# Performance work log

Hardware: AMD Instinct MI355X
Metric: run time of the kernel (lower is better)

## Reference

```python
import jax, jax.numpy as jnp
import numpy as np

D = 768      # embedding_dim
M = 3072     # mlp_dim
G = 4        # num_expert_groups
E = 8        # experts_per_group
KG = 2       # k_groups
KE = 4       # k_experts
EPS = 1e-6   # gate weight threshold from the torch module


def setup_inputs() -> dict:
    key = jax.random.key(0)
    ks = jax.random.split(key, 9)
    x = jax.random.normal(ks[0], (1, 1024, D), dtype=jnp.float32)
    Wg = jax.random.normal(ks[1], (D, G), dtype=jnp.float32) * 0.02
    bg = jax.random.normal(ks[2], (G,), dtype=jnp.float32) * 0.01
    We = jax.random.normal(ks[3], (G, D, E), dtype=jnp.float32) * 0.02
    be = jax.random.normal(ks[4], (G, E), dtype=jnp.float32) * 0.01
    W1 = jax.random.normal(ks[5], (G, E, D, M), dtype=jnp.float32) * 0.02
    b1 = jax.random.normal(ks[6], (G, E, M), dtype=jnp.float32) * 0.01
    W2 = jax.random.normal(ks[7], (G, E, M, D), dtype=jnp.float32) * 0.02
    b2 = jax.random.normal(ks[8], (G, E, D), dtype=jnp.float32) * 0.01
    return {"x": x, "Wg": Wg, "bg": bg, "We": We, "be": be,
            "W1": W1, "b1": b1, "W2": W2, "b2": b2}


def _topk_gates(logits, k):
    # top-k logits -> softmax over the k entries, then zero out weights < 1e-6
    top, idx = jax.lax.top_k(logits, k)
    gates = jax.nn.softmax(top, axis=-1)
    gates = jnp.where(gates >= EPS, gates, jnp.zeros_like(gates))
    return gates, idx


def reference(x, Wg, bg, We, be, W1, b1, W2, b2):
    orig_shape = x.shape
    xf = x.reshape(-1, D)  # [N, D]

    # ---- level 1: group gating (eval mode: clean logits, no noise) ----
    glog = xf @ Wg + bg                      # [N, G]
    ggates, gidx = _topk_gates(glog, KG)     # [N, KG]
    gw = jnp.einsum('nk,nkg->ng', ggates,
                    jax.nn.one_hot(gidx, G, dtype=xf.dtype))  # dense [N, G]

    # ---- level 2: expert gating within each group ----
    # computed densely for all groups; unselected groups get zero group weight
    elog = jnp.einsum('nd,gde->nge', xf, We) + be  # [N, G, E]
    egates, eidx = _topk_gates(elog, KE)            # [N, G, KE]
    ew = jnp.einsum('ngk,ngke->nge', egates,
                    jax.nn.one_hot(eidx, E, dtype=xf.dtype))  # dense [N, G, E]

    combine = gw[:, :, None] * ew  # [N, G, E] combine weights

    # ---- expert MLPs (dense compute, combine-weighted sum) ----
    y = jnp.zeros_like(xf)
    for g in range(G):  # small fixed loop over expert groups
        h = jax.nn.gelu(jnp.einsum('nd,edm->enm', xf, W1[g]) + b1[g][:, None, :],
                        approximate=False)               # [E, N, M]
        o = jnp.einsum('enm,emd->end', h, W2[g]) + b2[g][:, None, :]  # [E, N, D]
        y = y + jnp.einsum('end,ne->nd', o, combine[:, g, :])
    return y.reshape(orig_shape)
```

## Files before the change

### kernel.cpp

```cpp
#include <hip/hip_runtime.h>
#include <hip/hip_bf16.h>
#include <math.h>

#define NTOK 1024
#define DDIM 768
#define MDIM 3072
#define GN 4
#define EN 8
#define NEXP 32
#define NPAIR 8192
#define EPSW 1e-6f

typedef __attribute__((ext_vector_type(4))) float f32x4;
typedef __attribute__((ext_vector_type(4))) int   i32x4;
typedef __attribute__((ext_vector_type(4))) unsigned short u16x4;
typedef __attribute__((ext_vector_type(8))) __bf16 bf16x8;

__device__ __forceinline__ unsigned short f2bf(float f) {
  unsigned u = __builtin_bit_cast(unsigned, f);
  u += 0x7FFFu + ((u >> 16) & 1u);
  return (unsigned short)(u >> 16);
}

__global__ __launch_bounds__(256) void gating_kernel(
    const float* __restrict__ x, const float* __restrict__ Wg,
    const float* __restrict__ bg, const float* __restrict__ We,
    const float* __restrict__ be, int* __restrict__ counts,
    int* __restrict__ pair_e, float* __restrict__ pair_w)
{
  __shared__ float xr[DDIM];
  __shared__ float logits[36];
  const int n = blockIdx.x;
  const int tid = threadIdx.x;
  const float* xp = x + (size_t)n * DDIM;
  for (int d = tid; d < DDIM; d += 256) xr[d] = xp[d];
  __syncthreads();

  const int w = tid >> 6, lane = tid & 63;
  for (int j = 0; j < 9; ++j) {
    const int o = w + 4 * j;
    float s = 0.f;
    if (o < 4) {
      for (int d = lane; d < DDIM; d += 64) s += xr[d] * Wg[d * GN + o];
    } else {
      const int g = (o - 4) >> 3, e = (o - 4) & 7;
      const float* wp = We + (size_t)g * DDIM * EN + e;
      for (int d = lane; d < DDIM; d += 64) s += xr[d] * wp[d * EN];
    }
    for (int off = 32; off; off >>= 1) s += __shfl_xor(s, off);
    if (lane == 0) logits[o] = s + ((o < 4) ? bg[o] : be[o - 4]);
  }
  __syncthreads();

  if (tid == 0) {
    float gl[4];
    for (int i = 0; i < 4; ++i) gl[i] = logits[i];
    int i0 = 0;
    for (int i = 1; i < 4; ++i) if (gl[i] > gl[i0]) i0 = i;
    int i1 = -1;
    for (int i = 0; i < 4; ++i) {
      if (i == i0) continue;
      if (i1 < 0 || gl[i] > gl[i1]) i1 = i;
    }
    const float m = gl[i0];
    const float e1 = expf(gl[i1] - m);
    const float s2 = 1.f + e1;
    float gv[2] = { 1.f / s2, e1 / s2 };
    int gi[2] = { i0, i1 };
    for (int r = 0; r < 2; ++r) if (gv[r] < EPSW) gv[r] = 0.f;

    for (int r = 0; r < 2; ++r) {
      const int g = gi[r];
      float el[8];
      for (int e = 0; e < 8; ++e) el[e] = logits[4 + g * 8 + e];
      int sel[4];
      for (int q = 0; q < 4; ++q) {
        int best = -1;
        for (int e = 0; e < 8; ++e) {
          bool used = false;
          for (int p = 0; p < q; ++p) if (sel[p] == e) used = true;
          if (used) continue;
          if (best < 0 || el[e] > el[best]) best = e;
        }
        sel[q] = best;
      }
      const float mm = el[sel[0]];
      float ex[4]; float ss = 0.f;
      for (int q = 0; q < 4; ++q) { ex[q] = expf(el[sel[q]] - mm); ss += ex[q]; }
      for (int q = 0; q < 4; ++q) {
        float ew = ex[q] / ss;
        if (ew < EPSW) ew = 0.f;
        const int gbl = g * 8 + sel[q];
        const int j = r * 4 + q;
        pair_e[n * 8 + j] = gbl;
        pair_w[n * 8 + j] = gv[r] * ew;
        atomicAdd(&counts[gbl], 1);
      }
    }
  }
}

__global__ void scan_kernel(const int* __restrict__ counts, int* __restrict__ offsets)
{
  if (threadIdx.x == 0) {
    int a = 0;
    for (int i = 0; i < NEXP; ++i) { offsets[i] = a; a += counts[i]; }
  }
}

__global__ __launch_bounds__(256) void scatter_kernel(
    const float* __restrict__ x, const int* __restrict__ pair_e,
    const float* __restrict__ pair_w, const int* __restrict__ offsets,
    int* __restrict__ cursor, int* __restrict__ token_slots,
    float* __restrict__ slot_w, unsigned short* __restrict__ Xg)
{
  __shared__ int slots[8];
  const int n = blockIdx.x, tid = threadIdx.x;
  if (tid < 8) {
    const int e = pair_e[n * 8 + tid];
    const int s = offsets[e] + atomicAdd(&cursor[e], 1);
    slots[tid] = s;
    token_slots[n * 8 + tid] = s;
    slot_w[s] = pair_w[n * 8 + tid];
  }
  __syncthreads();
  const float* xp = x + (size_t)n * DDIM;
  for (int d = tid; d < DDIM; d += 256) {
    const unsigned short h = f2bf(xp[d]);
#pragma unroll
    for (int j = 0; j < 8; ++j) Xg[(size_t)slots[j] * DDIM + d] = h;
  }
}

template<int K, int NLD, int EPI>
__global__ __launch_bounds__(256) void moe_gemm(
    const unsigned short* __restrict__ A, const float* __restrict__ B,
    const float* __restrict__ bias, const int* __restrict__ counts,
    const int* __restrict__ offsets, const float* __restrict__ slot_w,
    unsigned short* __restrict__ Hout, float* __restrict__ Oout)
{
  const int ge = blockIdx.z;
  const int cnt = counts[ge];
  const int by = blockIdx.y;
  if (by * 128 >= cnt) return;
  const int off = offsets[ge];
  const int nb = blockIdx.x;

  __shared__ __align__(16) unsigned char ldsA[128 * 64];
  __shared__ __align__(16) unsigned char ldsB[128 * 64];

  const int tid = threadIdx.x;

  const int ar = tid >> 2;
  const int ac = tid & 3;
  int gr0 = by * 128 + ar;       if (gr0 >= cnt) gr0 = cnt - 1;
  int gr1 = by * 128 + ar + 64;  if (gr1 >= cnt) gr1 = cnt - 1;
  const unsigned short* aq0 = A + (size_t)(off + gr0) * K + ac * 8;
  const unsigned short* aq1 = A + (size_t)(off + gr1) * K + ac * 8;
  unsigned char* la0 = ldsA + ar * 64 + ((ac ^ ((ar >> 1) & 3)) * 16);
  unsigned char* la1 = ldsA + (ar + 64) * 64 + ((ac ^ ((ar >> 1) & 3)) * 16);

  const int kq = tid >> 5;
  const int ln = tid & 31;
  const float* bbase = B + (size_t)ge * K * NLD + (size_t)nb * 128;

  const int w = tid >> 6;
  const int lane = tid & 63;
  const int wr = (w >> 1) * 64;
  const int wc = (w & 1) * 64;
  const int l15 = lane & 15;
  const int l4 = lane >> 4;

  int aoff[4], boff[4];
#pragma unroll
  for (int mf = 0; mf < 4; ++mf) {
    const int r = wr + mf * 16 + l15;
    aoff[mf] = r * 64 + ((l4 ^ ((r >> 1) & 3)) * 16);
  }
#pragma unroll
  for (int nf = 0; nf < 4; ++nf) {
    const int c = wc + nf * 16 + l15;
    boff[nf] = c * 64 + ((l4 ^ ((c >> 1) & 3)) * 16);
  }

  f32x4 acc[4][4];
#pragma unroll
  for (int mf = 0; mf < 4; ++mf)
#pragma unroll
    for (int nf = 0; nf < 4; ++nf)
      acc[mf][nf] = (f32x4){0.f, 0.f, 0.f, 0.f};

  for (int kt = 0; kt < K / 32; ++kt) {
    const i32x4 av0 = *(const i32x4*)(aq0 + kt * 32);
    const i32x4 av1 = *(const i32x4*)(aq1 + kt * 32);
    *(i32x4*)la0 = av0;
    *(i32x4*)la1 = av1;
#pragma unroll
    for (int i = 0; i < 4; ++i) {
      const int n = ln + 32 * i;
      const float* bp = bbase + (size_t)(kt * 32 + kq * 4) * NLD + n;
      u16x4 p;
      p.x = f2bf(bp[0]);
      p.y = f2bf(bp[(size_t)NLD]);
      p.z = f2bf(bp[(size_t)2 * NLD]);
      p.w = f2bf(bp[(size_t)3 * NLD]);
      const int bo = n * 64 + (((kq >> 1) ^ ((n >> 1) & 3)) * 16) + ((kq & 1) * 8);
      *(u16x4*)(ldsB + bo) = p;
    }
    __syncthreads();

    bf16x8 afr[4], bfr[4];
#pragma unroll
    for (int mf = 0; mf < 4; ++mf)
      afr[mf] = __builtin_bit_cast(bf16x8, *(const i32x4*)(ldsA + aoff[mf]));
#pragma unroll
    for (int nf = 0; nf < 4; ++nf)
      bfr[nf] = __builtin_bit_cast(bf16x8, *(const i32x4*)(ldsB + boff[nf]));
#pragma unroll
    for (int mf = 0; mf < 4; ++mf)
#pragma unroll
      for (int nf = 0; nf < 4; ++nf)
        acc[mf][nf] = __builtin_amdgcn_mfma_f32_16x16x32_bf16(
            afr[mf], bfr[nf], acc[mf][nf], 0, 0, 0);
    __syncthreads();
  }

#pragma unroll
  for (int mf = 0; mf < 4; ++mf) {
    const int rbase = wr + mf * 16 + l4 * 4;
#pragma unroll
    for (int nf = 0; nf < 4; ++nf) {
      const int col = nb * 128 + wc + nf * 16 + l15;
      const float bv = bias[(size_t)ge * NLD + col];
#pragma unroll
      for (int j = 0; j < 4; ++j) {
        const int r = by * 128 + rbase + j;
        if (r < cnt) {
          const int slot = off + r;
          const float v = acc[mf][nf][j] + bv;
          if constexpr (EPI == 0) {
            const float gl = 0.5f * v * (1.f + erff(v * 0.70710678118654752f));
            Hout[(size_t)slot * NLD + col] = f2bf(gl);
          } else {
            Oout[(size_t)slot * NLD + col] = slot_w[slot] * v;
          }
        }
      }
    }
  }
}

__global__ __launch_bounds__(256) void gather_kernel(
    const int* __restrict__ token_slots, const float* __restrict__ O,
    float* __restrict__ y)
{
  const int n = blockIdx.x, tid = threadIdx.x;
  int s[8];
#pragma unroll
  for (int j = 0; j < 8; ++j) s[j] = token_slots[n * 8 + j];
  for (int d = tid; d < DDIM; d += 256) {
    float a = 0.f;
#pragma unroll
    for (int j = 0; j < 8; ++j) a += O[(size_t)s[j] * DDIM + d];
    y[(size_t)n * DDIM + d] = a;
  }
}

extern "C" void kernel_launch(void* const* d_in, const int* in_sizes, int n_in,
                              void* d_out, int out_size, void* d_ws, size_t ws_size,
                              hipStream_t stream)
{
  const float* x  = (const float*)d_in[0];
  const float* Wg = (const float*)d_in[1];
  const float* bg = (const float*)d_in[2];
  const float* We = (const float*)d_in[3];
  const float* be = (const float*)d_in[4];
  const float* W1 = (const float*)d_in[5];
  const float* b1 = (const float*)d_in[6];
  const float* W2 = (const float*)d_in[7];
  const float* b2 = (const float*)d_in[8];
  float* y = (float*)d_out;

  char* ws = (char*)d_ws;
  int*   counts      = (int*)(ws + 0);
  int*   offsets     = (int*)(ws + 256);
  int*   cursor      = (int*)(ws + 512);
  int*   pair_e      = (int*)(ws + 1024);
  float* pair_w      = (float*)(ws + 33792);
  int*   token_slots = (int*)(ws + 66560);
  float* slot_w      = (float*)(ws + 99328);
  unsigned short* Xg = (unsigned short*)(ws + 132096);
  unsigned short* H  = (unsigned short*)(ws + 12715008);
  float* O           = (float*)(ws + 63046656);

  hipMemsetAsync(ws, 0, 1024, stream);
  gating_kernel<<<NTOK, 256, 0, stream>>>(x, Wg, bg, We, be, counts, pair_e, pair_w);
  scan_kernel<<<1, 64, 0, stream>>>(counts, offsets);
  scatter_kernel<<<NTOK, 256, 0, stream>>>(x, pair_e, pair_w, offsets, cursor,
                                           token_slots, slot_w, Xg);
  moe_gemm<DDIM, MDIM, 0><<<dim3(MDIM / 128, 8, NEXP), 256, 0, stream>>>(
      Xg, W1, b1, counts, offsets, nullptr, H, nullptr);
  moe_gemm<MDIM, DDIM, 1><<<dim3(DDIM / 128, 8, NEXP), 256, 0, stream>>>(
      H, W2, b2, counts, offsets, slot_w, nullptr, O);
  gather_kernel<<<NTOK, 256, 0, stream>>>(token_slots, O, y);
}
```

Baseline: 583.3 us.

## Double-buffer MoE GEMM with async LDS loads and atomic output combine

After: 890.7 us. +52.7%, slower.

```diff
diff --git a/kernel.cpp b/kernel.cpp
--- a/kernel.cpp
+++ b/kernel.cpp
@@ -20,6 +20,12 @@
   unsigned u = __builtin_bit_cast(unsigned, f);
   u += 0x7FFFu + ((u >> 16) & 1u);
   return (unsigned short)(u >> 16);
+}
+
+__device__ __forceinline__ void gld_lds16(const void* g, void* l) {
+  __builtin_amdgcn_global_load_lds(
+      (const __attribute__((address_space(1))) void*)g,
+      (__attribute__((address_space(3))) void*)l, 16, 0, 0);
 }
 
 __global__ __launch_bounds__(256) void gating_kernel(
@@ -111,7 +117,7 @@
 __global__ __launch_bounds__(256) void scatter_kernel(
     const float* __restrict__ x, const int* __restrict__ pair_e,
     const float* __restrict__ pair_w, const int* __restrict__ offsets,
-    int* __restrict__ cursor, int* __restrict__ token_slots,
+    int* __restrict__ cursor, int* __restrict__ slot_tok,
     float* __restrict__ slot_w, unsigned short* __restrict__ Xg)
 {
   __shared__ int slots[8];
@@ -120,7 +126,7 @@
     const int e = pair_e[n * 8 + tid];
     const int s = offsets[e] + atomicAdd(&cursor[e], 1);
     slots[tid] = s;
-    token_slots[n * 8 + tid] = s;
+    slot_tok[s] = n;
     slot_w[s] = pair_w[n * 8 + tid];
   }
   __syncthreads();
@@ -133,43 +139,38 @@
 }
 
 template<int K, int NLD, int EPI>
-__global__ __launch_bounds__(256) void moe_gemm(
+__global__ __launch_bounds__(256, 3) void moe_gemm(
     const unsigned short* __restrict__ A, const float* __restrict__ B,
     const float* __restrict__ bias, const int* __restrict__ counts,
     const int* __restrict__ offsets, const float* __restrict__ slot_w,
-    unsigned short* __restrict__ Hout, float* __restrict__ Oout)
+    const int* __restrict__ slot_tok,
+    unsigned short* __restrict__ Hout, float* __restrict__ Yout)
 {
   const int ge = blockIdx.z;
   const int cnt = counts[ge];
-  const int by = blockIdx.y;
+  const int by = blockIdx.x;
   if (by * 128 >= cnt) return;
+  const int nb = blockIdx.y;
   const int off = offsets[ge];
-  const int nb = blockIdx.x;
-
-  __shared__ __align__(16) unsigned char ldsA[128 * 64];
-  __shared__ __align__(16) unsigned char ldsB[128 * 64];
-
   const int tid = threadIdx.x;
 
-  const int ar = tid >> 2;
-  const int ac = tid & 3;
-  int gr0 = by * 128 + ar;       if (gr0 >= cnt) gr0 = cnt - 1;
-  int gr1 = by * 128 + ar + 64;  if (gr1 >= cnt) gr1 = cnt - 1;
-  const unsigned short* aq0 = A + (size_t)(off + gr0) * K + ac * 8;
-  const unsigned short* aq1 = A + (size_t)(off + gr1) * K + ac * 8;
-  unsigned char* la0 = ldsA + ar * 64 + ((ac ^ ((ar >> 1) & 3)) * 16);
-  unsigned char* la1 = ldsA + (ar + 64) * 64 + ((ac ^ ((ar >> 1) & 3)) * 16);
-
-  const int kq = tid >> 5;
-  const int ln = tid & 31;
-  const float* bbase = B + (size_t)ge * K * NLD + (size_t)nb * 128;
-
-  const int w = tid >> 6;
-  const int lane = tid & 63;
-  const int wr = (w >> 1) * 64;
-  const int wc = (w & 1) * 64;
-  const int l15 = lane & 15;
-  const int l4 = lane >> 4;
+  __shared__ __align__(16) unsigned char ldsA[2][8192];
+  __shared__ __align__(16) unsigned char ldsB[2][8192];
+
+  const int ar = tid >> 2, ac = tid & 3;
+  const int sc = ac ^ ((ar >> 1) & 3);
+  int gr0 = by * 128 + ar;      if (gr0 >= cnt) gr0 = cnt - 1;
+  int gr1 = by * 128 + ar + 64; if (gr1 >= cnt) gr1 = cnt - 1;
+  const unsigned short* asrc0 = A + (size_t)(off + gr0) * K + sc * 8;
+  const unsigned short* asrc1 = A + (size_t)(off + gr1) * K + sc * 8;
+
+  const int kq = tid >> 5, ln = tid & 31;
+  const float* bsrc = B + (size_t)ge * K * NLD + (size_t)(kq * 4) * NLD
+                        + (size_t)nb * 128 + ln;
+
+  const int w = tid >> 6, lane = tid & 63;
+  const int wr = (w >> 1) * 64, wc = (w & 1) * 64;
+  const int l15 = lane & 15, l4 = lane >> 4;
 
   int aoff[4], boff[4];
 #pragma unroll
@@ -190,79 +191,99 @@
     for (int nf = 0; nf < 4; ++nf)
       acc[mf][nf] = (f32x4){0.f, 0.f, 0.f, 0.f};
 
-  for (int kt = 0; kt < K / 32; ++kt) {
-    const i32x4 av0 = *(const i32x4*)(aq0 + kt * 32);
-    const i32x4 av1 = *(const i32x4*)(aq1 + kt * 32);
-    *(i32x4*)la0 = av0;
-    *(i32x4*)la1 = av1;
-#pragma unroll
-    for (int i = 0; i < 4; ++i) {
-      const int n = ln + 32 * i;
-      const float* bp = bbase + (size_t)(kt * 32 + kq * 4) * NLD + n;
-      u16x4 p;
-      p.x = f2bf(bp[0]);
-      p.y = f2bf(bp[(size_t)NLD]);
-      p.z = f2bf(bp[(size_t)2 * NLD]);
-      p.w = f2bf(bp[(size_t)3 * NLD]);
-      const int bo = n * 64 + (((kq >> 1) ^ ((n >> 1) & 3)) * 16) + ((kq & 1) * 8);
-      *(u16x4*)(ldsB + bo) = p;
-    }
-    __syncthreads();
-
+  float bs[16];
+
+  gld_lds16(asrc0, &ldsA[0][tid * 16]);
+  gld_lds16(asrc1, &ldsA[0][4096 + tid * 16]);
+  asrc0 += 32; asrc1 += 32;
+#pragma unroll
+  for (int i = 0; i < 4; ++i)
+#pragma unroll
+    for (int r = 0; r < 4; ++r)
+      bs[i * 4 + r] = bsrc[(size_t)r * NLD + 32 * i];
+  bsrc += (size_t)32 * NLD;
+#pragma unroll
+  for (int i = 0; i < 4; ++i) {
+    const int n = ln + 32 * i;
+    u16x4 p = { f2bf(bs[i*4+0]), f2bf(bs[i*4+1]), f2bf(bs[i*4+2]), f2bf(bs[i*4+3]) };
+    *(u16x4*)(&ldsB[0][n * 64 + (((kq >> 1) ^ ((n >> 1) & 3)) * 16) + ((kq & 1) * 8)]) = p;
+  }
+  __syncthreads();
+
+  const int NT = K / 32;
+  for (int t = 0; t < NT; ++t) {
+    const int cur = t & 1;
+    if (t + 1 < NT) {
+      gld_lds16(asrc0, &ldsA[cur ^ 1][tid * 16]);
+      gld_lds16(asrc1, &ldsA[cur ^ 1][4096 + tid * 16]);
+      asrc0 += 32; asrc1 += 32;
+#pragma unroll
+      for (int i = 0; i < 4; ++i)
+#pragma unroll
+        for (int r = 0; r < 4; ++r)
+          bs[i * 4 + r] = bsrc[(size_t)r * NLD + 32 * i];
+      bsrc += (size_t)32 * NLD;
+    }
     bf16x8 afr[4], bfr[4];
 #pragma unroll
     for (int mf = 0; mf < 4; ++mf)
-      afr[mf] = __builtin_bit_cast(bf16x8, *(const i32x4*)(ldsA + aoff[mf]));
+      afr[mf] = __builtin_bit_cast(bf16x8, *(const i32x4*)(&ldsA[cur][aoff[mf]]));
 #pragma unroll
     for (int nf = 0; nf < 4; ++nf)
-      bfr[nf] = __builtin_bit_cast(bf16x8, *(const i32x4*)(ldsB + boff[nf]));
+      bfr[nf] = __builtin_bit_cast(bf16x8, *(const i32x4*)(&ldsB[cur][boff[nf]]));
 #pragma unroll
     for (int mf = 0; mf < 4; ++mf)
 #pragma unroll
       for (int nf = 0; nf < 4; ++nf)
         acc[mf][nf] = __builtin_amdgcn_mfma_f32_16x16x32_bf16(
             afr[mf], bfr[nf], acc[mf][nf], 0, 0, 0);
+    if (t + 1 < NT) {
+#pragma unroll
+      for (int i = 0; i < 4; ++i) {
+        const int n = ln + 32 * i;
+        u16x4 p = { f2bf(bs[i*4+0]), f2bf(bs[i*4+1]), f2bf(bs[i*4+2]), f2bf(bs[i*4+3]) };
+        *(u16x4*)(&ldsB[cur ^ 1][n * 64 + (((kq >> 1) ^ ((n >> 1) & 3)) * 16) + ((kq & 1) * 8)]) = p;
+      }
+    }
     __syncthreads();
   }
 
 #pragma unroll
   for (int mf = 0; mf < 4; ++mf) {
-    const int rbase = wr + mf * 16 + l4 * 4;
-#pragma unroll
-    for (int nf = 0; nf < 4; ++nf) {
-      const int col = nb * 128 + wc + nf * 16 + l15;
-      const float bv = bias[(size_t)ge * NLD + col];
+    const int rbase = by * 128 + wr + mf * 16 + l4 * 4;
+    if constexpr (EPI == 0) {
+#pragma unroll
+      for (int nf = 0; nf < 4; ++nf) {
+        const int col = nb * 128 + wc + nf * 16 + l15;
+        const float bv = bias[(size_t)ge * NLD + col];
+#pragma unroll
+        for (int j = 0; j < 4; ++j) {
+          const int r = rbase + j;
+          if (r < cnt) {
+            const int slot = off + r;
+            const float v = acc[mf][nf][j] + bv;
+            const float gl = 0.5f * v * (1.f + erff(v * 0.70710678118654752f));
+            Hout[(size_t)slot * NLD + col] = f2bf(gl);
+          }
+        }
+      }
+    } else {
 #pragma unroll
       for (int j = 0; j < 4; ++j) {
-        const int r = by * 128 + rbase + j;
+        const int r = rbase + j;
         if (r < cnt) {
           const int slot = off + r;
-          const float v = acc[mf][nf][j] + bv;
-          if constexpr (EPI == 0) {
-            const float gl = 0.5f * v * (1.f + erff(v * 0.70710678118654752f));
-            Hout[(size_t)slot * NLD + col] = f2bf(gl);
-          } else {
-            Oout[(size_t)slot * NLD + col] = slot_w[slot] * v;
+          const float sw = slot_w[slot];
+          const int tok = slot_tok[slot];
+#pragma unroll
+          for (int nf = 0; nf < 4; ++nf) {
+            const int col = nb * 128 + wc + nf * 16 + l15;
+            const float v = acc[mf][nf][j] + bias[(size_t)ge * NLD + col];
+            atomicAdd(&Yout[(size_t)tok * DDIM + col], sw * v);
           }
         }
       }
     }
-  }
-}
-
-__global__ __launch_bounds__(256) void gather_kernel(
-    const int* __restrict__ token_slots, const float* __restrict__ O,
-    float* __restrict__ y)
-{
-  const int n = blockIdx.x, tid = threadIdx.x;
-  int s[8];
-#pragma unroll
-  for (int j = 0; j < 8; ++j) s[j] = token_slots[n * 8 + j];
-  for (int d = tid; d < DDIM; d += 256) {
-    float a = 0.f;
-#pragma unroll
-    for (int j = 0; j < 8; ++j) a += O[(size_t)s[j] * DDIM + d];
-    y[(size_t)n * DDIM + d] = a;
   }
 }
 
@@ -282,25 +303,24 @@
   float* y = (float*)d_out;
 
   char* ws = (char*)d_ws;
-  int*   counts      = (int*)(ws + 0);
-  int*   offsets     = (int*)(ws + 256);
-  int*   cursor      = (int*)(ws + 512);
-  int*   pair_e      = (int*)(ws + 1024);
-  float* pair_w      = (float*)(ws + 33792);
-  int*   token_slots = (int*)(ws + 66560);
-  float* slot_w      = (float*)(ws + 99328);
+  int*   counts   = (int*)(ws + 0);
+  int*   offsets  = (int*)(ws + 256);
+  int*   cursor   = (int*)(ws + 512);
+  int*   pair_e   = (int*)(ws + 1024);
+  float* pair_w   = (float*)(ws + 33792);
+  int*   slot_tok = (int*)(ws + 66560);
+  float* slot_w   = (float*)(ws + 99328);
   unsigned short* Xg = (unsigned short*)(ws + 132096);
   unsigned short* H  = (unsigned short*)(ws + 12715008);
-  float* O           = (float*)(ws + 63046656);
 
   hipMemsetAsync(ws, 0, 1024, stream);
+  hipMemsetAsync(y, 0, (size_t)NTOK * DDIM * sizeof(float), stream);
   gating_kernel<<<NTOK, 256, 0, stream>>>(x, Wg, bg, We, be, counts, pair_e, pair_w);
   scan_kernel<<<1, 64, 0, stream>>>(counts, offsets);
   scatter_kernel<<<NTOK, 256, 0, stream>>>(x, pair_e, pair_w, offsets, cursor,
-                                           token_slots, slot_w, Xg);
-  moe_gemm<DDIM, MDIM, 0><<<dim3(MDIM / 128, 8, NEXP), 256, 0, stream>>>(
-      Xg, W1, b1, counts, offsets, nullptr, H, nullptr);
-  moe_gemm<MDIM, DDIM, 1><<<dim3(DDIM / 128, 8, NEXP), 256, 0, stream>>>(
-      H, W2, b2, counts, offsets, slot_w, nullptr, O);
-  gather_kernel<<<NTOK, 256, 0, stream>>>(token_slots, O, y);
-}
+                                           slot_tok, slot_w, Xg);
+  moe_gemm<DDIM, MDIM, 0><<<dim3(8, MDIM / 128, NEXP), 256, 0, stream>>>(
+      Xg, W1, b1, counts, offsets, nullptr, nullptr, H, nullptr);
+  moe_gemm<MDIM, DDIM, 1><<<dim3(8, DDIM / 128, NEXP), 256, 0, stream>>>(
+      H, W2, b2, counts, offsets, slot_w, slot_tok, nullptr, y);
+}
```
